# Kernel tuning notes

Measured on AMD Instinct MI355X. Metric: run time of the kernel, lower is better.

Reference implementation:

```python
import jax, jax.numpy as jnp
import numpy as np

N = 100000
E = 1600000
DIN = 128
DH = 128
DOUT = 32
G = 64
EPS = 1e-5


def setup_inputs() -> dict:
    key = jax.random.key(0)
    ks = jax.random.split(key, 12)
    x = jax.random.normal(ks[0], (N, DIN), dtype=jnp.float32)
    edge_index = jax.random.randint(ks[1], (2, E), 0, N, dtype=jnp.int64)
    batch = jnp.sort(jax.random.randint(ks[2], (N,), 0, G, dtype=jnp.int64))
    # GCNConv weights (glorot-ish) + zero bias
    W1 = jax.random.normal(ks[3], (DIN, DH), dtype=jnp.float32) * (2.0 / (DIN + DH)) ** 0.5
    b1 = jnp.zeros((DH,), jnp.float32)
    W2 = jax.random.normal(ks[4], (DH, DH), dtype=jnp.float32) * (2.0 / (DH + DH)) ** 0.5
    b2 = jnp.zeros((DH,), jnp.float32)
    # BatchNorm affine params
    g1 = jnp.ones((DH,), jnp.float32); be1 = jnp.zeros((DH,), jnp.float32)
    g2 = jnp.ones((DH,), jnp.float32); be2 = jnp.zeros((DH,), jnp.float32)
    # Linear heads: kaiming normal fan_in relu, bias=0.001
    fw1 = jax.random.normal(ks[5], (DH, DH), dtype=jnp.float32) * (2.0 / DH) ** 0.5
    fb1 = jnp.full((DH,), 0.001, jnp.float32)
    fw2 = jax.random.normal(ks[6], (DH, DOUT), dtype=jnp.float32) * (2.0 / DH) ** 0.5
    fb2 = jnp.full((DOUT,), 0.001, jnp.float32)
    return dict(x=x, edge_index=edge_index, batch=batch, W1=W1, b1=b1, W2=W2, b2=b2,
                g1=g1, be1=be1, g2=g2, be2=be2, fw1=fw1, fb1=fb1, fw2=fw2, fb2=fb2)


def _gcn(x, src, dst, dinv, W, b):
    h = x @ W  # [N, F]
    norm = dinv[src] * dinv[dst]  # [E+N]
    agg = jax.ops.segment_sum(h[src] * norm[:, None], dst, num_segments=N)
    return agg + b


def _bn(h, gamma, beta):
    mu = h.mean(axis=0)
    var = h.var(axis=0)  # biased, matches torch BN training mode
    return (h - mu) * jax.lax.rsqrt(var + EPS) * gamma + beta


def reference(x, edge_index, batch, W1, b1, W2, b2, g1, be1, g2, be2, fw1, fb1, fw2, fb2):
    # add self-loops (PyG GCNConv default)
    loops = jnp.arange(N, dtype=edge_index.dtype)
    src = jnp.concatenate([edge_index[0], loops])
    dst = jnp.concatenate([edge_index[1], loops])
    deg = jax.ops.segment_sum(jnp.ones_like(dst, dtype=x.dtype), dst, num_segments=N)
    dinv = jnp.where(deg > 0, jax.lax.rsqrt(deg), 0.0)

    h = jax.nn.relu(_bn(_gcn(x, src, dst, dinv, W1, b1), g1, be1))
    h = jax.nn.relu(_bn(_gcn(h, src, dst, dinv, W2, b2), g2, be2))

    # global mean pool over graph ids
    sums = jax.ops.segment_sum(h, batch, num_segments=G)
    cnt = jax.ops.segment_sum(jnp.ones((N,), h.dtype), batch, num_segments=G)
    pooled = sums / jnp.maximum(cnt, 1.0)[:, None]  # [G, DH]

    z = jax.nn.relu(pooled @ fw1 + fb1)
    return jax.nn.softmax(z @ fw2 + fb2, axis=1)
```

## Files before the change

### kernel.cpp

```cpp
#include <hip/hip_runtime.h>
#include <hip/hip_bf16.h>
#include <stdint.h>

#define NN 100000
#define NE 1600000
#define DH 128
#define DOUT 32
#define NG 64
#define EPS 1e-5f

#define SCAN_BLK 1024
#define SCAN_NB ((NN + SCAN_BLK - 1) / SCAN_BLK)
#define NBUCKET 32
#define NRANGE 8
#define RANGE_SZ (NN / NRANGE)

#define PREP_COUNT_BLKS 1024
#define PREP_GB_BLKS ((NN + 255) / 256)
#define PREP_PW_BLKS 128

#define AGG_BLOCKS 4096
#define NCHUNK 32768

typedef __attribute__((ext_vector_type(8))) unsigned short ushort8;
typedef __attribute__((ext_vector_type(8))) short bfv8;
typedef __attribute__((ext_vector_type(4))) float f32x4;
typedef __attribute__((ext_vector_type(4))) int intv4;
typedef __attribute__((ext_vector_type(2))) unsigned int uintv2;

__device__ __forceinline__ float b2f(unsigned short u) {
    return __uint_as_float(((unsigned int)u) << 16);
}
__device__ __forceinline__ unsigned int f2b(float f) {
    unsigned int u = __float_as_uint(f);
    return (u + 0x7fffu + ((u >> 16) & 1u)) >> 16;
}
__device__ __forceinline__ float blo(unsigned int v) { return __uint_as_float(v << 16); }
__device__ __forceinline__ float bhi(unsigned int v) { return __uint_as_float(v & 0xffff0000u); }


__global__ void k_prep(const int* __restrict__ ei_dst, int* __restrict__ cnt,
                       const int* __restrict__ batch, int* __restrict__ gfirst, int* __restrict__ glast,
                       const float* __restrict__ W1, const float* __restrict__ W2,
                       unsigned short* __restrict__ WT1, unsigned short* __restrict__ WT2) {
    int bid = blockIdx.x;
    int t = threadIdx.x;
    if (bid < PREP_COUNT_BLKS) {
        int range = bid & (NRANGE - 1);
        int lo = range * RANGE_SZ, hi = lo + RANGE_SZ;
        int i = (bid >> 3) * 256 + t;
        int stride = (PREP_COUNT_BLKS >> 3) * 256;
        const intv4* d4 = reinterpret_cast<const intv4*>(ei_dst);
        for (int e = i; e < NE / 4; e += stride) {
            intv4 d = __builtin_nontemporal_load(d4 + e);
            if (d.x >= lo && d.x < hi) atomicAdd(&cnt[d.x], 1);
            if (d.y >= lo && d.y < hi) atomicAdd(&cnt[d.y], 1);
            if (d.z >= lo && d.z < hi) atomicAdd(&cnt[d.z], 1);
            if (d.w >= lo && d.w < hi) atomicAdd(&cnt[d.w], 1);
        }
    } else if (bid < PREP_COUNT_BLKS + PREP_GB_BLKS) {
        int i = (bid - PREP_COUNT_BLKS) * 256 + t;
        if (i < NN) {
            int g = batch[i];
            if (i == 0 || batch[i - 1] != g) gfirst[g] = i;
            if (i == NN - 1 || batch[i + 1] != g) glast[g] = i + 1;
        }
    } else {
        int i = (bid - PREP_COUNT_BLKS - PREP_GB_BLKS) * 256 + t;
        int sel = i >> 14;
        int j = i & 16383;
        int k = j >> 7, n = j & 127;
        const float* W = sel ? W2 : W1;
        unsigned short* WT = sel ? WT2 : WT1;
        WT[n * 128 + k] = (unsigned short)f2b(W[j]);
    }
}


__global__ void k_scan_partial(const int* __restrict__ cnt, int* __restrict__ bsum) {
    __shared__ int sdata[256];
    int blk = blockIdx.x, t = threadIdx.x;
    int base = blk * SCAN_BLK + t * 4;
    int s = 0;
#pragma unroll
    for (int q = 0; q < 4; q++) { int idx = base + q; if (idx < NN) s += cnt[idx]; }
    sdata[t] = s; __syncthreads();
    for (int o = 128; o; o >>= 1) { if (t < o) sdata[t] += sdata[t + o]; __syncthreads(); }
    if (t == 0) bsum[blk] = sdata[0];
}

__global__ void k_scan_final(int* __restrict__ cnt, const int* __restrict__ bsum,
                             int* __restrict__ rowptr, float* __restrict__ dinv,
                             const int* __restrict__ first, const int* __restrict__ last,
                             int* __restrict__ gcnt) {
    __shared__ int sdata[256];
    __shared__ int stop[128];
    __shared__ int sbase;
    int blk = blockIdx.x, t = threadIdx.x;

    if (t < 128) stop[t] = (t < SCAN_NB) ? bsum[t] : 0;
    __syncthreads();
    for (int o = 1; o < 128; o <<= 1) {
        int add = (t < 128 && t >= o) ? stop[t - o] : 0;
        __syncthreads();
        if (t < 128) stop[t] += add;
        __syncthreads();
    }
    if (t == 0) sbase = (blk > 0) ? stop[blk - 1] : 0;
    if (blk == 0) {
        if (t == 127) rowptr[NN] = stop[127];
        if (t < NG) gcnt[t] = last[t] - first[t];
    }
    __syncthreads();

    int base = blk * SCAN_BLK + t * 4;
    int v[4]; int s = 0;
#pragma unroll
    for (int q = 0; q < 4; q++) { int idx = base + q; v[q] = (idx < NN) ? cnt[idx] : 0; s += v[q]; }
    sdata[t] = s; __syncthreads();
    for (int o = 1; o < 256; o <<= 1) {
        int add = (t >= o) ? sdata[t - o] : 0;
        __syncthreads();
        sdata[t] += add;
        __syncthreads();
    }
    int offset = sbase + sdata[t] - s;
#pragma unroll
    for (int q = 0; q < 4; q++) {
        int idx = base + q;
        if (idx < NN) {
            rowptr[idx] = offset;
            cnt[idx] = offset;
            dinv[idx] = rsqrtf((float)(v[q] + 1));
            offset += v[q];
        }
    }
}

__global__ void k_fill(const int* __restrict__ ei, int* __restrict__ cursor, int* __restrict__ csr) {
    int range = blockIdx.x & (NRANGE - 1);
    int lo = range * RANGE_SZ, hi = lo + RANGE_SZ;
    int i = (blockIdx.x >> 3) * blockDim.x + threadIdx.x;
    int stride = (gridDim.x >> 3) * blockDim.x;
    const intv4* s4 = reinterpret_cast<const intv4*>(ei);
    const intv4* d4 = reinterpret_cast<const intv4*>(ei + NE);
    for (int e = i; e < NE / 4; e += stride) {
        intv4 s = __builtin_nontemporal_load(s4 + e);
        intv4 d = __builtin_nontemporal_load(d4 + e);
        if (d.x >= lo && d.x < hi) csr[atomicAdd(&cursor[d.x], 1)] = s.x;
        if (d.y >= lo && d.y < hi) csr[atomicAdd(&cursor[d.y], 1)] = s.y;
        if (d.z >= lo && d.z < hi) csr[atomicAdd(&cursor[d.z], 1)] = s.z;
        if (d.w >= lo && d.w < hi) csr[atomicAdd(&cursor[d.w], 1)] = s.w;
    }
}


template <bool BN, typename AT>
__global__ __launch_bounds__(256) void k_gemm(const AT* __restrict__ A, const unsigned short* __restrict__ WTg,
                                              unsigned short* __restrict__ C, const float* __restrict__ rowscale,
                                              const float* __restrict__ scale, const float* __restrict__ shift) {
    __shared__ unsigned char lds[65536];
    unsigned char* As = lds;
    unsigned char* Ws = lds + 32768;
    int row0 = blockIdx.x * 128;
    int t = threadIdx.x;
    int l = t & 63;
    int w = t >> 6;

    if constexpr (sizeof(AT) == 4) {
#pragma unroll
        for (int q = 0; q < 16; q++) {
            int idx = q * 256 + t;
            int r = idx >> 5, c4 = idx & 31;
            float4 v = make_float4(0.f, 0.f, 0.f, 0.f);
            if (row0 + r < NN) v = reinterpret_cast<const float4*>(A)[(size_t)(row0 + r) * 32 + c4];
            ushort4 u;
            u.x = (unsigned short)f2b(v.x);
            u.y = (unsigned short)f2b(v.y);
            u.z = (unsigned short)f2b(v.z);
            u.w = (unsigned short)f2b(v.w);
            int off = r * 256 + ((c4 * 8) ^ ((r & 7) << 4));
            *reinterpret_cast<ushort4*>(As + off) = u;
        }
    } else {
#pragma unroll
        for (int q = 0; q < 8; q++) {
            int idx = q * 256 + t;
            int r = idx >> 4, c8 = idx & 15;
            ushort8 v = (ushort8)0;
            if (row0 + r < NN) v = reinterpret_cast<const ushort8*>(A)[(size_t)(row0 + r) * 16 + c8];
            ushort8 u;
#pragma unroll
            for (int j = 0; j < 8; j++) {
                float f = b2f(v[j]);
                if (BN) { int k = c8 * 8 + j; f = fmaxf(f * scale[k] + shift[k], 0.f); }
                u[j] = (unsigned short)f2b(f);
            }
            int off = r * 256 + ((c8 * 16) ^ ((r & 7) << 4));
            *reinterpret_cast<ushort8*>(As + off) = u;
        }
    }
#pragma unroll
    for (int q = 0; q < 8; q++) {
        int idx = q * 256 + t;
        int n = idx >> 4, c8 = idx & 15;
        ushort8 v = reinterpret_cast<const ushort8*>(WTg)[idx];
        int off = n * 256 + ((c8 * 16) ^ ((n & 7) << 4));
        *reinterpret_cast<ushort8*>(Ws + off) = v;
    }
    __syncthreads();

    f32x4 acc[2][8];
#pragma unroll
    for (int m = 0; m < 2; m++)
#pragma unroll
        for (int n = 0; n < 8; n++) acc[m][n] = (f32x4)0.f;

    int lrow = l & 15;
    int kbyte0 = (l >> 4) * 16;
#pragma unroll
    for (int kt = 0; kt < 4; kt++) {
        int kb = kt * 64 + kbyte0;
        bfv8 a[2];
#pragma unroll
        for (int m = 0; m < 2; m++) {
            int r = w * 32 + m * 16 + lrow;
            a[m] = *reinterpret_cast<const bfv8*>(As + r * 256 + (kb ^ ((r & 7) << 4)));
        }
        bfv8 b[8];
#pragma unroll
        for (int n = 0; n < 8; n++) {
            int r = n * 16 + lrow;
            b[n] = *reinterpret_cast<const bfv8*>(Ws + r * 256 + (kb ^ ((r & 7) << 4)));
        }
#pragma unroll
        for (int m = 0; m < 2; m++)
#pragma unroll
            for (int n = 0; n < 8; n++)
                acc[m][n] = __builtin_amdgcn_mfma_f32_16x16x32_bf16(a[m], b[n], acc[m][n], 0, 0, 0);
    }

#pragma unroll
    for (int m = 0; m < 2; m++) {
#pragma unroll
        for (int rr = 0; rr < 4; rr++) {
            int grow = row0 + w * 32 + m * 16 + (l >> 4) * 4 + rr;
            if (grow < NN) {
                float rs = rowscale[grow];
#pragma unroll
                for (int n = 0; n < 8; n++) {
                    int col = n * 16 + (l & 15);
                    C[(size_t)grow * DH + col] = (unsigned short)f2b(acc[m][n][rr] * rs);
                }
            }
        }
    }
}


__global__ __launch_bounds__(128) void k_aggregate(const unsigned short* __restrict__ h, const int* __restrict__ rowptr,
                                                   const int* __restrict__ csr, const float* __restrict__ dinv,
                                                   unsigned short* __restrict__ agg, float* __restrict__ stats) {
    int lane = threadIdx.x & 63;
    int wv = threadIdx.x >> 6;
    int half = lane >> 5;
    int sl = lane & 31;
    const uintv2* h64 = reinterpret_cast<const uintv2*>(h);
    uintv2* agg64 = reinterpret_cast<uintv2*>(agg);
    int wid = blockIdx.x * 2 + wv;
    int nw = gridDim.x * 2;

    float s0 = 0.f, s1 = 0.f, s2 = 0.f, s3 = 0.f;
    float q0 = 0.f, q1 = 0.f, q2 = 0.f, q3 = 0.f;

    for (int c = wid; c < NCHUNK; c += nw) {
        long long tlo = ((long long)c * NE) / NCHUNK;
        long long thi = (c == NCHUNK - 1) ? (long long)NE + 1 : (((long long)(c + 1) * NE) / NCHUNK);
        int thii = (int)thi;

        int lo = 0, hi = NN;
        while (lo < hi) {
            int mid = (lo + hi) >> 1;
            if (rowptr[mid] < (int)tlo) lo = mid + 1; else hi = mid;
        }

        for (int i = lo; i < NN; i++) {
            int row = rowptr[i];
            if (row >= thii) break;
            int end = rowptr[i + 1];
            int len = end - row;
            float di = dinv[i];
            float a0 = 0.f, a1 = 0.f, a2 = 0.f, a3 = 0.f;
            if (half == 0) {
                uintv2 sv = h64[(size_t)i * 32 + sl];
                a0 = blo(sv.x); a1 = bhi(sv.x); a2 = blo(sv.y); a3 = bhi(sv.y);
            }
            int hc = (len + 1 - half) >> 1;
            int tt = 0;
            for (; tt + 4 <= hc; tt += 4) {
                int eA = row + (tt << 1) + half;
                int n0 = csr[eA], n1 = csr[eA + 2], n2 = csr[eA + 4], n3 = csr[eA + 6];
                uintv2 v0 = h64[(size_t)n0 * 32 + sl];
                uintv2 v1 = h64[(size_t)n1 * 32 + sl];
                uintv2 v2 = h64[(size_t)n2 * 32 + sl];
                uintv2 v3 = h64[(size_t)n3 * 32 + sl];
                a0 += blo(v0.x); a1 += bhi(v0.x); a2 += blo(v0.y); a3 += bhi(v0.y);
                a0 += blo(v1.x); a1 += bhi(v1.x); a2 += blo(v1.y); a3 += bhi(v1.y);
                a0 += blo(v2.x); a1 += bhi(v2.x); a2 += blo(v2.y); a3 += bhi(v2.y);
                a0 += blo(v3.x); a1 += bhi(v3.x); a2 += blo(v3.y); a3 += bhi(v3.y);
            }
            for (; tt < hc; tt++) {
                int e = row + (tt << 1) + half;
                int n = csr[e];
                uintv2 v = h64[(size_t)n * 32 + sl];
                a0 += blo(v.x); a1 += bhi(v.x); a2 += blo(v.y); a3 += bhi(v.y);
            }
            a0 += __shfl_xor(a0, 32);
            a1 += __shfl_xor(a1, 32);
            a2 += __shfl_xor(a2, 32);
            a3 += __shfl_xor(a3, 32);
            a0 *= di; a1 *= di; a2 *= di; a3 *= di;
            if (half == 0) {
                uintv2 o;
                o.x = f2b(a0) | (f2b(a1) << 16);
                o.y = f2b(a2) | (f2b(a3) << 16);
                agg64[(size_t)i * 32 + sl] = o;
                s0 += a0; q0 += a0 * a0;
                s1 += a1; q1 += a1 * a1;
                s2 += a2; q2 += a2 * a2;
                s3 += a3; q3 += a3 * a3;
            }
        }
    }

    if (half == 0) {
        float* b = stats + (size_t)(wid & (NBUCKET - 1)) * 256;
        atomicAdd(&b[sl * 4 + 0], s0);
        atomicAdd(&b[sl * 4 + 1], s1);
        atomicAdd(&b[sl * 4 + 2], s2);
        atomicAdd(&b[sl * 4 + 3], s3);
        atomicAdd(&b[128 + sl * 4 + 0], q0);
        atomicAdd(&b[128 + sl * 4 + 1], q1);
        atomicAdd(&b[128 + sl * 4 + 2], q2);
        atomicAdd(&b[128 + sl * 4 + 3], q3);
    }
}

__global__ void k_bnparams(const float* __restrict__ stats, const float* __restrict__ gamma,
                           const float* __restrict__ beta, float* __restrict__ scale, float* __restrict__ shift) {
    int j = threadIdx.x;
    float su = 0.f, sq = 0.f;
    for (int b = 0; b < NBUCKET; b++) { su += stats[b * 256 + j]; sq += stats[b * 256 + 128 + j]; }
    float mu = su * (1.f / NN);
    float var = sq * (1.f / NN) - mu * mu;
    float rs = rsqrtf(var + EPS);
    float sc = rs * gamma[j];
    scale[j] = sc;
    shift[j] = beta[j] - mu * sc;
}


#define POOL_CHUNK 64

__global__ __launch_bounds__(64) void k_pool(const unsigned short* __restrict__ agg, const int* __restrict__ batch,
                                             const float* __restrict__ scale, const float* __restrict__ shift,
                                             float* __restrict__ pooled) {
    int j = threadIdx.x;
    const unsigned int* a32 = reinterpret_cast<const unsigned int*>(agg);
    int n0 = blockIdx.x * POOL_CHUNK;
    int n1 = n0 + POOL_CHUNK; if (n1 > NN) n1 = NN;
    float sc0 = scale[j * 2], sh0 = shift[j * 2];
    float sc1 = scale[j * 2 + 1], sh1 = shift[j * 2 + 1];
    int gcur = batch[n0];
    float acc0 = 0.f, acc1 = 0.f;
    for (int i = n0; i < n1; i++) {
        int g = batch[i];
        if (g != gcur) {
            atomicAdd(&pooled[(size_t)gcur * DH + j * 2], acc0);
            atomicAdd(&pooled[(size_t)gcur * DH + j * 2 + 1], acc1);
            acc0 = acc1 = 0.f; gcur = g;
        }
        unsigned int v = a32[(size_t)i * 64 + j];
        acc0 += fmaxf(blo(v) * sc0 + sh0, 0.f);
        acc1 += fmaxf(bhi(v) * sc1 + sh1, 0.f);
    }
    atomicAdd(&pooled[(size_t)gcur * DH + j * 2], acc0);
    atomicAdd(&pooled[(size_t)gcur * DH + j * 2 + 1], acc1);
}


__global__ __launch_bounds__(128) void k_head(const float* __restrict__ pooled, const int* __restrict__ gcnt,
                                              const float* __restrict__ fw1, const float* __restrict__ fb1,
                                              const float* __restrict__ fw2, const float* __restrict__ fb2,
                                              float* __restrict__ out) {
    __shared__ float p[DH];
    __shared__ float z[DH];
    int g = blockIdx.x;
    int j = threadIdx.x;
    float cnt = (float)max(gcnt[g], 1);
    p[j] = pooled[(size_t)g * DH + j] / cnt;
    __syncthreads();
    float a = fb1[j];
    for (int k = 0; k < DH; k++) a += p[k] * fw1[k * DH + j];
    z[j] = fmaxf(a, 0.f);
    __syncthreads();
    if (j < DOUT) {
        float l = fb2[j];
        for (int k = 0; k < DH; k++) l += z[k] * fw2[k * DOUT + j];
        float m = l;
        for (int o = 16; o; o >>= 1) m = fmaxf(m, __shfl_xor(m, o, 32));
        float e = expf(l - m);
        float s = e;
        for (int o = 16; o; o >>= 1) s += __shfl_xor(s, o, 32);
        out[(size_t)g * DOUT + j] = e / s;
    }
}


static inline char* align256p(char* p) {
    return (char*)(((uintptr_t)p + 255) & ~(uintptr_t)255);
}

extern "C" void kernel_launch(void* const* d_in, const int* in_sizes, int n_in,
                              void* d_out, int out_size, void* d_ws, size_t ws_size,
                              hipStream_t stream) {
    const float* x     = (const float*)d_in[0];
    const int*   ei    = (const int*)d_in[1];
    const int*   batch = (const int*)d_in[2];
    const float* W1    = (const float*)d_in[3];
    const float* W2    = (const float*)d_in[5];
    const float* g1    = (const float*)d_in[7];
    const float* be1   = (const float*)d_in[8];
    const float* g2    = (const float*)d_in[9];
    const float* be2   = (const float*)d_in[10];
    const float* fw1   = (const float*)d_in[11];
    const float* fb1   = (const float*)d_in[12];
    const float* fw2   = (const float*)d_in[13];
    const float* fb2   = (const float*)d_in[14];
    float* out = (float*)d_out;

    char* w = (char*)d_ws;
    unsigned short* hbuf = (unsigned short*)w;  w += (size_t)NN * DH * 2;
    unsigned short* abuf = (unsigned short*)w;  w += (size_t)NN * DH * 2;
    int*   csr    = (int*)w;    w += (size_t)NE * 4;
    int*   rowptr = (int*)w;    w += (size_t)(NN + 1) * 4;  w = align256p(w);
    float* dinv   = (float*)w;  w += (size_t)NN * 4;
    int*   bsum   = (int*)w;    w += 512 * 4;
    float* scale1 = (float*)w;  w += DH * 4;
    float* shift1 = (float*)w;  w += DH * 4;
    float* scale2 = (float*)w;  w += DH * 4;
    float* shift2 = (float*)w;  w += DH * 4;
    unsigned short* WT1g = (unsigned short*)w;  w += (size_t)DH * DH * 2;
    unsigned short* WT2g = (unsigned short*)w;  w += (size_t)DH * DH * 2;
    w = align256p(w);
    char* zstart  = w;
    int*   cnt    = (int*)w;    w += (size_t)NN * 4;
    int*   gfirst = (int*)w;    w += 64 * 4;
    int*   glast  = (int*)w;    w += 64 * 4;
    int*   gcnt   = (int*)w;    w += 64 * 4;
    float* stats1 = (float*)w;  w += (size_t)NBUCKET * 256 * 4;
    float* stats2 = (float*)w;  w += (size_t)NBUCKET * 256 * 4;
    float* pooled = (float*)w;  w += (size_t)NG * DH * 4;
    size_t zbytes = (size_t)(w - zstart);
    size_t need = (size_t)(w - (char*)d_ws);
    if (ws_size < need) return;

    hipMemsetAsync(zstart, 0, zbytes, stream);

    k_prep<<<PREP_COUNT_BLKS + PREP_GB_BLKS + PREP_PW_BLKS, 256, 0, stream>>>(
        ei + NE, cnt, batch, gfirst, glast, W1, W2, WT1g, WT2g);
    k_scan_partial<<<SCAN_NB, 256, 0, stream>>>(cnt, bsum);
    k_scan_final<<<SCAN_NB, 256, 0, stream>>>(cnt, bsum, rowptr, dinv, gfirst, glast, gcnt);
    k_fill<<<1024, 256, 0, stream>>>(ei, cnt, csr);

    int gemm_grid = (NN + 127) / 128;

    k_gemm<false, float><<<gemm_grid, 256, 0, stream>>>(x, WT1g, hbuf, dinv, nullptr, nullptr);
    k_aggregate<<<AGG_BLOCKS, 128, 0, stream>>>(hbuf, rowptr, csr, dinv, abuf, stats1);
    k_bnparams<<<1, 128, 0, stream>>>(stats1, g1, be1, scale1, shift1);

    k_gemm<true, unsigned short><<<gemm_grid, 256, 0, stream>>>(abuf, WT2g, hbuf, dinv, scale1, shift1);
    k_aggregate<<<AGG_BLOCKS, 128, 0, stream>>>(hbuf, rowptr, csr, dinv, abuf, stats2);
    k_bnparams<<<1, 128, 0, stream>>>(stats2, g2, be2, scale2, shift2);

    int pool_grid = (NN + POOL_CHUNK - 1) / POOL_CHUNK;
    k_pool<<<pool_grid, 64, 0, stream>>>(abuf, batch, scale2, shift2, pooled);
    k_head<<<NG, 128, 0, stream>>>(pooled, gcnt, fw1, fb1, fw2, fb2, out);
}
```

Measured before the change: 443.3 us.

## Store features in 8 column slices and aggregate each slice separately

```diff
diff --git a/kernel.cpp b/kernel.cpp
--- a/kernel.cpp
+++ b/kernel.cpp
@@ -20,13 +20,13 @@
 #define PREP_PW_BLKS 128
 
 #define AGG_BLOCKS 4096
-#define NCHUNK 32768
+#define AGG_NCHUNK 4096
+#define NSLICE 8
 
 typedef __attribute__((ext_vector_type(8))) unsigned short ushort8;
 typedef __attribute__((ext_vector_type(8))) short bfv8;
 typedef __attribute__((ext_vector_type(4))) float f32x4;
 typedef __attribute__((ext_vector_type(4))) int intv4;
-typedef __attribute__((ext_vector_type(2))) unsigned int uintv2;
 
 __device__ __forceinline__ float b2f(unsigned short u) {
     return __uint_as_float(((unsigned int)u) << 16);
@@ -188,7 +188,10 @@
             int idx = q * 256 + t;
             int r = idx >> 4, c8 = idx & 15;
             ushort8 v = (ushort8)0;
-            if (row0 + r < NN) v = reinterpret_cast<const ushort8*>(A)[(size_t)(row0 + r) * 16 + c8];
+            if (row0 + r < NN)
+                v = *reinterpret_cast<const ushort8*>(
+                        (const unsigned short*)A + (size_t)(c8 >> 1) * NN * 16 +
+                        (size_t)(row0 + r) * 16 + (c8 & 1) * 8);
             ushort8 u;
 #pragma unroll
             for (int j = 0; j < 8; j++) {
@@ -249,8 +252,8 @@
                 float rs = rowscale[grow];
 #pragma unroll
                 for (int n = 0; n < 8; n++) {
-                    int col = n * 16 + (l & 15);
-                    C[(size_t)grow * DH + col] = (unsigned short)f2b(acc[m][n][rr] * rs);
+                    C[(size_t)n * NN * 16 + (size_t)grow * 16 + (l & 15)] =
+                        (unsigned short)f2b(acc[m][n][rr] * rs);
                 }
             }
         }
@@ -263,19 +266,19 @@
                                                    unsigned short* __restrict__ agg, float* __restrict__ stats) {
     int lane = threadIdx.x & 63;
     int wv = threadIdx.x >> 6;
-    int half = lane >> 5;
-    int sl = lane & 31;
-    const uintv2* h64 = reinterpret_cast<const uintv2*>(h);
-    uintv2* agg64 = reinterpret_cast<uintv2*>(agg);
-    int wid = blockIdx.x * 2 + wv;
-    int nw = gridDim.x * 2;
-
-    float s0 = 0.f, s1 = 0.f, s2 = 0.f, s3 = 0.f;
-    float q0 = 0.f, q1 = 0.f, q2 = 0.f, q3 = 0.f;
-
-    for (int c = wid; c < NCHUNK; c += nw) {
-        long long tlo = ((long long)c * NE) / NCHUNK;
-        long long thi = (c == NCHUNK - 1) ? (long long)NE + 1 : (((long long)(c + 1) * NE) / NCHUNK);
+    int slot = lane >> 3;
+    int f = lane & 7;
+    int slice = blockIdx.x & (NSLICE - 1);
+    const unsigned int* h32 = reinterpret_cast<const unsigned int*>(h) + (size_t)slice * NN * 8;
+    unsigned int* agg32 = reinterpret_cast<unsigned int*>(agg) + (size_t)slice * NN * 8;
+    int ws = (blockIdx.x >> 3) * 2 + wv;
+    int nws = (gridDim.x >> 3) * 2;
+
+    float s0 = 0.f, s1 = 0.f, q0 = 0.f, q1 = 0.f;
+
+    for (int c = ws; c < AGG_NCHUNK; c += nws) {
+        long long tlo = ((long long)c * NE) / AGG_NCHUNK;
+        long long thi = (c == AGG_NCHUNK - 1) ? (long long)NE + 1 : (((long long)(c + 1) * NE) / AGG_NCHUNK);
         int thii = (int)thi;
 
         int lo = 0, hi = NN;
@@ -290,59 +293,44 @@
             int end = rowptr[i + 1];
             int len = end - row;
             float di = dinv[i];
-            float a0 = 0.f, a1 = 0.f, a2 = 0.f, a3 = 0.f;
-            if (half == 0) {
-                uintv2 sv = h64[(size_t)i * 32 + sl];
-                a0 = blo(sv.x); a1 = bhi(sv.x); a2 = blo(sv.y); a3 = bhi(sv.y);
-            }
-            int hc = (len + 1 - half) >> 1;
-            int tt = 0;
-            for (; tt + 4 <= hc; tt += 4) {
-                int eA = row + (tt << 1) + half;
-                int n0 = csr[eA], n1 = csr[eA + 2], n2 = csr[eA + 4], n3 = csr[eA + 6];
-                uintv2 v0 = h64[(size_t)n0 * 32 + sl];
-                uintv2 v1 = h64[(size_t)n1 * 32 + sl];
-                uintv2 v2 = h64[(size_t)n2 * 32 + sl];
-                uintv2 v3 = h64[(size_t)n3 * 32 + sl];
-                a0 += blo(v0.x); a1 += bhi(v0.x); a2 += blo(v0.y); a3 += bhi(v0.y);
-                a0 += blo(v1.x); a1 += bhi(v1.x); a2 += blo(v1.y); a3 += bhi(v1.y);
-                a0 += blo(v2.x); a1 += bhi(v2.x); a2 += blo(v2.y); a3 += bhi(v2.y);
-                a0 += blo(v3.x); a1 += bhi(v3.x); a2 += blo(v3.y); a3 += bhi(v3.y);
-            }
-            for (; tt < hc; tt++) {
-                int e = row + (tt << 1) + half;
-                int n = csr[e];
-                uintv2 v = h64[(size_t)n * 32 + sl];
-                a0 += blo(v.x); a1 += bhi(v.x); a2 += blo(v.y); a3 += bhi(v.y);
-            }
-            a0 += __shfl_xor(a0, 32);
-            a1 += __shfl_xor(a1, 32);
-            a2 += __shfl_xor(a2, 32);
-            a3 += __shfl_xor(a3, 32);
-            a0 *= di; a1 *= di; a2 *= di; a3 *= di;
-            if (half == 0) {
-                uintv2 o;
-                o.x = f2b(a0) | (f2b(a1) << 16);
-                o.y = f2b(a2) | (f2b(a3) << 16);
-                agg64[(size_t)i * 32 + sl] = o;
+            float a0 = 0.f, a1 = 0.f;
+            if (slot == 0) {
+                unsigned int sv = h32[(size_t)i * 8 + f];
+                a0 = blo(sv); a1 = bhi(sv);
+            }
+            int tt = slot;
+            for (; tt + 8 < len; tt += 16) {
+                int n0 = __builtin_nontemporal_load(&csr[row + tt]);
+                int n1 = __builtin_nontemporal_load(&csr[row + tt + 8]);
+                unsigned int v0 = h32[(size_t)n0 * 8 + f];
+                unsigned int v1 = h32[(size_t)n1 * 8 + f];
+                a0 += blo(v0) + blo(v1);
+                a1 += bhi(v0) + bhi(v1);
+            }
+            if (tt < len) {
+                int n = __builtin_nontemporal_load(&csr[row + tt]);
+                unsigned int v = h32[(size_t)n * 8 + f];
+                a0 += blo(v); a1 += bhi(v);
+            }
+            a0 += __shfl_xor(a0, 8);  a1 += __shfl_xor(a1, 8);
+            a0 += __shfl_xor(a0, 16); a1 += __shfl_xor(a1, 16);
+            a0 += __shfl_xor(a0, 32); a1 += __shfl_xor(a1, 32);
+            a0 *= di; a1 *= di;
+            if (slot == 0) {
+                agg32[(size_t)i * 8 + f] = f2b(a0) | (f2b(a1) << 16);
                 s0 += a0; q0 += a0 * a0;
                 s1 += a1; q1 += a1 * a1;
-                s2 += a2; q2 += a2 * a2;
-                s3 += a3; q3 += a3 * a3;
-            }
-        }
-    }
-
-    if (half == 0) {
-        float* b = stats + (size_t)(wid & (NBUCKET - 1)) * 256;
-        atomicAdd(&b[sl * 4 + 0], s0);
-        atomicAdd(&b[sl * 4 + 1], s1);
-        atomicAdd(&b[sl * 4 + 2], s2);
-        atomicAdd(&b[sl * 4 + 3], s3);
-        atomicAdd(&b[128 + sl * 4 + 0], q0);
-        atomicAdd(&b[128 + sl * 4 + 1], q1);
-        atomicAdd(&b[128 + sl * 4 + 2], q2);
-        atomicAdd(&b[128 + sl * 4 + 3], q3);
+            }
+        }
+    }
+
+    if (slot == 0) {
+        float* b = stats + (size_t)(ws & (NBUCKET - 1)) * 256;
+        int j = slice * 16 + f * 2;
+        atomicAdd(&b[j], s0);
+        atomicAdd(&b[j + 1], s1);
+        atomicAdd(&b[128 + j], q0);
+        atomicAdd(&b[128 + j + 1], q1);
     }
 }
 
@@ -366,7 +354,7 @@
                                              const float* __restrict__ scale, const float* __restrict__ shift,
                                              float* __restrict__ pooled) {
     int j = threadIdx.x;
-    const unsigned int* a32 = reinterpret_cast<const unsigned int*>(agg);
+    const unsigned int* a32 = reinterpret_cast<const unsigned int*>(agg) + (size_t)(j >> 3) * NN * 8 + (j & 7);
     int n0 = blockIdx.x * POOL_CHUNK;
     int n1 = n0 + POOL_CHUNK; if (n1 > NN) n1 = NN;
     float sc0 = scale[j * 2], sh0 = shift[j * 2];
@@ -380,7 +368,7 @@
             atomicAdd(&pooled[(size_t)gcur * DH + j * 2 + 1], acc1);
             acc0 = acc1 = 0.f; gcur = g;
         }
-        unsigned int v = a32[(size_t)i * 64 + j];
+        unsigned int v = a32[(size_t)i * 8];
         acc0 += fmaxf(blo(v) * sc0 + sh0, 0.f);
         acc1 += fmaxf(bhi(v) * sc1 + sh1, 0.f);
     }
```

Measured after the change: 861.2 us. +94.3%, slower.
